# Performance work log

Hardware: AMD Instinct MI355X
Metric: run time of the kernel (lower is better)

## Reference

```python
import jax, jax.numpy as jnp
import numpy as np

D = 768; H = 6; HD = D // H; DFF = 2048
L = 512; S = 1024; B = 8
EPS = 1e-5
SCALE = 1.0 / float(np.sqrt(2 * D // H))  # fused q/k head_dim = 2*D/H (Conditional-DETR attention)


def _ln(x, g, b):
    m = x.mean(-1, keepdims=True)
    v = ((x - m) ** 2).mean(-1, keepdims=True)
    return (x - m) / jnp.sqrt(v + EPS) * g + b


def _lin(x, w, b):  # w: (out, in) torch convention
    return jnp.einsum('lbd,ed->lbe', x, w) + b


def _fuse(c, p):  # channel-concat per head: (L,B,D)x2 -> (L,B,H,2*HD)
    Lx, Bx, _ = c.shape
    c = c.reshape(Lx, Bx, H, HD)
    p = p.reshape(Lx, Bx, H, HD)
    return jnp.concatenate([c, p], axis=-1)


def _attn(q, k, v, ow, ob):
    # q:(L,B,H,2HD) k:(S,B,H,2HD) v:(S,B,D); out_proj maps vdim->vdim
    Lx, Bx = q.shape[0], q.shape[1]
    Sx = k.shape[0]
    vh = v.reshape(Sx, Bx, H, HD)
    scores = jnp.einsum('lbhd,sbhd->bhls', q * SCALE, k)
    w = jax.nn.softmax(scores, axis=-1)
    o = jnp.einsum('bhls,sbhe->lbhe', w, vh).reshape(Lx, Bx, D)
    return _lin(o, ow, ob), w.mean(axis=1)  # head-averaged attn weights (B,L,S)


def setup_inputs() -> dict:
    key = jax.random.key(0)
    ks = iter(jax.random.split(key, 64))
    d = {}
    d['tgt'] = jax.random.normal(next(ks), (L, B, D), jnp.float32)
    d['memory'] = jax.random.normal(next(ks), (S, B, D), jnp.float32)
    d['tgt_pos'] = jax.random.normal(next(ks), (L, B, D), jnp.float32)
    d['memory_pos'] = jax.random.normal(next(ks), (S, B, D), jnp.float32)
    d['tgt_pos2'] = jax.random.normal(next(ks), (L, B, D), jnp.float32)

    def W(shape):
        return jax.random.normal(next(ks), shape, jnp.float32) * 0.02

    for pre in ('sa', 'ca'):
        for nm in ('qc', 'qp', 'kc', 'kp', 'v', 'o'):
            d[f'{pre}_{nm}_w'] = W((D, D))
            d[f'{pre}_{nm}_b'] = jnp.zeros((D,), jnp.float32)
    d['ff1_w'] = W((DFF, D)); d['ff1_b'] = jnp.zeros((DFF,), jnp.float32)
    d['ff2_w'] = W((D, DFF)); d['ff2_b'] = jnp.zeros((D,), jnp.float32)
    for i in (1, 2, 3):
        d[f'ln{i}_g'] = jnp.ones((D,), jnp.float32)
        d[f'ln{i}_b'] = jnp.zeros((D,), jnp.float32)
    return d


def reference(tgt, memory, tgt_pos, memory_pos, tgt_pos2,
              sa_qc_w, sa_qc_b, sa_qp_w, sa_qp_b, sa_kc_w, sa_kc_b, sa_kp_w, sa_kp_b,
              sa_v_w, sa_v_b, sa_o_w, sa_o_b,
              ca_qc_w, ca_qc_b, ca_qp_w, ca_qp_b, ca_kc_w, ca_kc_b, ca_kp_w, ca_kp_b,
              ca_v_w, ca_v_b, ca_o_w, ca_o_b,
              ff1_w, ff1_b, ff2_w, ff2_b,
              ln1_g, ln1_b, ln2_g, ln2_b, ln3_g, ln3_b):
    # --- self attention (dropout = identity at inference) ---
    q = _fuse(_lin(tgt_pos, sa_qc_w, sa_qc_b), _lin(tgt, sa_qp_w, sa_qp_b))
    k = _fuse(_lin(tgt_pos, sa_kc_w, sa_kc_b), _lin(tgt, sa_kp_w, sa_kp_b))
    v = _lin(tgt, sa_v_w, sa_v_b)
    t2, self_att = _attn(q, k, v, sa_o_w, sa_o_b)
    t = _ln(tgt + t2, ln1_g, ln1_b)
    # --- cross attention ---
    q = _fuse(_lin(tgt_pos, ca_qc_w, ca_qc_b), _lin(t + tgt_pos2, ca_qp_w, ca_qp_b))
    k = _fuse(_lin(memory, ca_kc_w, ca_kc_b), _lin(memory_pos, ca_kp_w, ca_kp_b))
    v = _lin(memory_pos, ca_v_w, ca_v_b)
    t2, att = _attn(q, k, v, ca_o_w, ca_o_b)
    t = _ln(t + t2, ln2_g, ln2_b)
    # --- FFN + post-norm ---
    t2 = _lin(jax.nn.relu(_lin(t, ff1_w, ff1_b)), ff2_w, ff2_b)
    t = _ln(t + t2, ln3_g, ln3_b)
    return (t, att, self_att)
```

## Files before the change

### kernel.cpp

```cpp
#include <hip/hip_runtime.h>


typedef __bf16 bf16;
typedef __attribute__((ext_vector_type(8))) __bf16 bf16x8;
typedef __attribute__((ext_vector_type(4))) float f32x4;

#define D_MODEL 768
#define NH 6
#define HD 128
#define ROWSTRIDE (8 * D_MODEL)

__device__ inline void swz_xyz(int& x, int& y, int& z) {
    const int nx = gridDim.x, ny = gridDim.y;
    const int n = nx * ny * gridDim.z;
    const int flat = blockIdx.x + nx * (blockIdx.y + ny * blockIdx.z);
    const int t = (flat & 7) * (n >> 3) + (flat >> 3);
    x = t % nx;
    const int r = t / nx;
    y = r % ny;
    z = r / ny;
}

__device__ __forceinline__ void gld16(const bf16* g, bf16* l) {
    __builtin_amdgcn_global_load_lds(
        (const __attribute__((address_space(1))) unsigned int*)g,
        (__attribute__((address_space(3))) unsigned int*)l, 16, 0, 0);
}

__device__ inline bf16x8 ld8f(const float* p) {
    f32x4 a = *(const f32x4*)p, b = *(const f32x4*)(p + 4);
    bf16x8 r;
#pragma unroll
    for (int i = 0; i < 4; i++) { r[i] = (bf16)a[i]; r[i + 4] = (bf16)b[i]; }
    return r;
}
__device__ inline bf16x8 ld8bf(const bf16* p, const float* q) {
    bf16x8 x = *(const bf16x8*)p;
    f32x4 a = *(const f32x4*)q, b = *(const f32x4*)(q + 4);
    bf16x8 r;
#pragma unroll
    for (int i = 0; i < 4; i++) { r[i] = (bf16)((float)x[i] + a[i]); r[i + 4] = (bf16)((float)x[i + 4] + b[i]); }
    return r;
}
__device__ inline bf16x8 ld8ff(const float* p, const float* q) {
    f32x4 a = *(const f32x4*)p, b = *(const f32x4*)(p + 4);
    f32x4 c = *(const f32x4*)q, d = *(const f32x4*)(q + 4);
    bf16x8 r;
#pragma unroll
    for (int i = 0; i < 4; i++) { r[i] = (bf16)(a[i] + c[i]); r[i + 4] = (bf16)(b[i] + d[i]); }
    return r;
}

struct CvtJob { const float* src; const bf16* add; bf16* dst; int nvec; };
struct CvtJobs { CvtJob j[12]; };

__global__ __launch_bounds__(256) void cvt_multi(CvtJobs jobs)
{
    const CvtJob jb = jobs.j[blockIdx.y];
    const int stride = gridDim.x * 256;
    if (jb.add) {
        for (int i = blockIdx.x * 256 + threadIdx.x; i < jb.nvec; i += stride)
            *(bf16x8*)(jb.dst + (size_t)i * 8) = ld8bf(jb.add + (size_t)i * 8, jb.src + (size_t)i * 8);
    } else {
        for (int i = blockIdx.x * 256 + threadIdx.x; i < jb.nvec; i += stride)
            *(bf16x8*)(jb.dst + (size_t)i * 8) = ld8f(jb.src + (size_t)i * 8);
    }
}

struct JobB { const bf16* A; const bf16* W; const float* bias; bf16* C; int relu; };
struct JobsB { JobB j[5]; };

__global__ __launch_bounds__(256) void gemm_bb(
    JobsB jobs, int lda, int ldw, int ldc, int K)
{
    __shared__ __align__(16) bf16 As[128 * 32];
    __shared__ __align__(16) bf16 Bs[128 * 32];
    int bx, by, bz;
    swz_xyz(bx, by, bz);
    const JobB jb = jobs.j[bz];
    const int bm = by * 128, bn = bx * 128;
    const int tid = threadIdx.x;
    const int wave = tid >> 6, lane = tid & 63;
    const int wm = (wave >> 1) * 64, wn = (wave & 1) * 64;
    const int quad = lane >> 4, m16 = lane & 15;
    const int crow = lane >> 2, ccol = (lane & 3) * 8;
    const bf16* a0 = jb.A + (size_t)(bm + wave * 32 + crow) * lda + ccol;
    const bf16* a1 = a0 + (size_t)16 * lda;
    const bf16* w0 = jb.W + (size_t)(bn + wave * 32 + crow) * ldw + ccol;
    const bf16* w1 = w0 + (size_t)16 * ldw;
    bf16* lA = As + wave * 1024;
    bf16* lB = Bs + wave * 1024;
    f32x4 acc[4][4] = {};
    for (int k0 = 0; k0 < K; k0 += 32) {
        gld16(a0 + k0, lA);
        gld16(a1 + k0, lA + 512);
        gld16(w0 + k0, lB);
        gld16(w1 + k0, lB + 512);
        __syncthreads();
        bf16x8 af[4], bfr[4];
#pragma unroll
        for (int i = 0; i < 4; i++) {
            af[i]  = *(const bf16x8*)&As[(wm + i * 16 + m16) * 32 + quad * 8];
            bfr[i] = *(const bf16x8*)&Bs[(wn + i * 16 + m16) * 32 + quad * 8];
        }
#pragma unroll
        for (int i = 0; i < 4; i++)
#pragma unroll
            for (int j = 0; j < 4; j++)
                acc[i][j] = __builtin_amdgcn_mfma_f32_16x16x32_bf16(af[i], bfr[j], acc[i][j], 0, 0, 0);
        __syncthreads();
    }
#pragma unroll
    for (int j = 0; j < 4; j++) {
        const int col = bn + wn + j * 16 + m16;
        const float bv = jb.bias[col];
#pragma unroll
        for (int i = 0; i < 4; i++)
#pragma unroll
            for (int r = 0; r < 4; r++) {
                const int row = bm + wm + i * 16 + quad * 4 + r;
                float val = acc[i][j][r] + bv;
                if (jb.relu) val = fmaxf(val, 0.f);
                jb.C[(size_t)row * ldc + col] = (bf16)val;
            }
    }
}

__global__ __launch_bounds__(256) void gemm_sk_bb(
    const bf16* __restrict__ A, int lda, const bf16* __restrict__ W, int ldw,
    float* __restrict__ Cp, size_t cstride, int ldc, int Ks)
{
    __shared__ __align__(16) bf16 As[128 * 32];
    __shared__ __align__(16) bf16 Bs[128 * 32];
    int bx, by, bz;
    swz_xyz(bx, by, bz);
    const int bm = by * 128, bn = bx * 128;
    const int kbase = bz * Ks;
    const int tid = threadIdx.x;
    const int wave = tid >> 6, lane = tid & 63;
    const int wm = (wave >> 1) * 64, wn = (wave & 1) * 64;
    const int quad = lane >> 4, m16 = lane & 15;
    const int crow = lane >> 2, ccol = (lane & 3) * 8;
    const bf16* a0 = A + (size_t)(bm + wave * 32 + crow) * lda + kbase + ccol;
    const bf16* a1 = a0 + (size_t)16 * lda;
    const bf16* w0 = W + (size_t)(bn + wave * 32 + crow) * ldw + kbase + ccol;
    const bf16* w1 = w0 + (size_t)16 * ldw;
    bf16* lA = As + wave * 1024;
    bf16* lB = Bs + wave * 1024;
    f32x4 acc[4][4] = {};
    for (int k0 = 0; k0 < Ks; k0 += 32) {
        gld16(a0 + k0, lA);
        gld16(a1 + k0, lA + 512);
        gld16(w0 + k0, lB);
        gld16(w1 + k0, lB + 512);
        __syncthreads();
        bf16x8 af[4], bfr[4];
#pragma unroll
        for (int i = 0; i < 4; i++) {
            af[i]  = *(const bf16x8*)&As[(wm + i * 16 + m16) * 32 + quad * 8];
            bfr[i] = *(const bf16x8*)&Bs[(wn + i * 16 + m16) * 32 + quad * 8];
        }
#pragma unroll
        for (int i = 0; i < 4; i++)
#pragma unroll
            for (int j = 0; j < 4; j++)
                acc[i][j] = __builtin_amdgcn_mfma_f32_16x16x32_bf16(af[i], bfr[j], acc[i][j], 0, 0, 0);
        __syncthreads();
    }
    float* out = Cp + (size_t)bz * cstride;
#pragma unroll
    for (int j = 0; j < 4; j++) {
        const int col = bn + wn + j * 16 + m16;
#pragma unroll
        for (int i = 0; i < 4; i++)
#pragma unroll
            for (int r = 0; r < 4; r++) {
                const int row = bm + wm + i * 16 + quad * 4 + r;
                out[(size_t)row * ldc + col] = acc[i][j][r];
            }
    }
}

__global__ __launch_bounds__(256) void gemm_sk3(
    const float* __restrict__ A, const float* __restrict__ A2, int lda,
    const float* __restrict__ W, int ldw,
    float* __restrict__ Cp, size_t cstride, int ldc, int Ks)
{
    __shared__ __align__(16) bf16 As[128][40];
    __shared__ __align__(16) bf16 Bs[128][40];
    int bx, by, bz;
    swz_xyz(bx, by, bz);
    const int bm = by * 128, bn = bx * 128;
    const int kbase = bz * Ks;
    const int tid = threadIdx.x;
    const int wave = tid >> 6, lane = tid & 63;
    const int wm = (wave >> 1) * 64, wn = (wave & 1) * 64;
    const int quad = lane >> 4, m16 = lane & 15;
    const int srow = tid >> 2, scol = (tid & 3) * 8;
    f32x4 acc[4][4] = {};
    const size_t aoff0 = (size_t)(bm + srow) * lda + kbase + scol;
    const size_t aoff1 = aoff0 + (size_t)64 * lda;
    const size_t woff0 = (size_t)(bn + srow) * ldw + kbase + scol;
    const size_t woff1 = woff0 + (size_t)64 * ldw;
    bf16x8 a0, a1, b0, b1;
    a0 = ld8ff(A + aoff0, A2 + aoff0);
    a1 = ld8ff(A + aoff1, A2 + aoff1);
    b0 = ld8f(W + woff0);
    b1 = ld8f(W + woff1);
    for (int k0 = 0; k0 < Ks; k0 += 32) {
        *(bf16x8*)&As[srow][scol]      = a0;
        *(bf16x8*)&As[srow + 64][scol] = a1;
        *(bf16x8*)&Bs[srow][scol]      = b0;
        *(bf16x8*)&Bs[srow + 64][scol] = b1;
        __syncthreads();
        const int kn = k0 + 32;
        if (kn < Ks) {
            a0 = ld8ff(A + aoff0 + kn, A2 + aoff0 + kn);
            a1 = ld8ff(A + aoff1 + kn, A2 + aoff1 + kn);
            b0 = ld8f(W + woff0 + kn);
            b1 = ld8f(W + woff1 + kn);
        }
        bf16x8 af[4], bfr[4];
#pragma unroll
        for (int i = 0; i < 4; i++) {
            af[i]  = *(const bf16x8*)&As[wm + i * 16 + m16][quad * 8];
            bfr[i] = *(const bf16x8*)&Bs[wn + i * 16 + m16][quad * 8];
        }
#pragma unroll
        for (int i = 0; i < 4; i++)
#pragma unroll
            for (int j = 0; j < 4; j++)
                acc[i][j] = __builtin_amdgcn_mfma_f32_16x16x32_bf16(af[i], bfr[j], acc[i][j], 0, 0, 0);
        __syncthreads();
    }
    float* out = Cp + (size_t)bz * cstride;
#pragma unroll
    for (int j = 0; j < 4; j++) {
        const int col = bn + wn + j * 16 + m16;
#pragma unroll
        for (int i = 0; i < 4; i++)
#pragma unroll
            for (int r = 0; r < 4; r++) {
                const int row = bm + wm + i * 16 + quad * 4 + r;
                out[(size_t)row * ldc + col] = acc[i][j][r];
            }
    }
}

__global__ __launch_bounds__(256) void attn_scores(
    const bf16* __restrict__ qc, const bf16* __restrict__ qp,
    const bf16* __restrict__ kc, const bf16* __restrict__ kp,
    bf16* __restrict__ scores, int Lq, int S, float scale)
{
    __shared__ __align__(16) bf16 As[128 * 32];
    __shared__ __align__(16) bf16 Bs[128 * 32];
    int bx, by, bz;
    swz_xyz(bx, by, bz);
    const int bh = bz;
    const int b = bh / NH, h = bh % NH;
    const int bm = by * 128, bn = bx * 128;
    const int tid = threadIdx.x;
    const int wave = tid >> 6, lane = tid & 63;
    const int wm = (wave >> 1) * 64, wn = (wave & 1) * 64;
    const int quad = lane >> 4, m16 = lane & 15;
    const int crow = lane >> 2, ccol = (lane & 3) * 8;
    const size_t hb = (size_t)b * D_MODEL + h * HD;
    const size_t ar0 = (size_t)(bm + wave * 32 + crow) * ROWSTRIDE + hb + ccol;
    const size_t ar1 = ar0 + (size_t)16 * ROWSTRIDE;
    const size_t br0 = (size_t)(bn + wave * 32 + crow) * ROWSTRIDE + hb + ccol;
    const size_t br1 = br0 + (size_t)16 * ROWSTRIDE;
    bf16* lA = As + wave * 1024;
    bf16* lB = Bs + wave * 1024;
    f32x4 acc[4][4] = {};
    for (int k0 = 0; k0 < 256; k0 += 32) {
        const bf16* qsrc = (k0 < 128) ? qc : qp;
        const bf16* ksrc = (k0 < 128) ? kc : kp;
        const int kcol = k0 & 127;
        gld16(qsrc + ar0 + kcol, lA);
        gld16(qsrc + ar1 + kcol, lA + 512);
        gld16(ksrc + br0 + kcol, lB);
        gld16(ksrc + br1 + kcol, lB + 512);
        __syncthreads();
        bf16x8 af[4], bfr[4];
#pragma unroll
        for (int i = 0; i < 4; i++) {
            af[i]  = *(const bf16x8*)&As[(wm + i * 16 + m16) * 32 + quad * 8];
            bfr[i] = *(const bf16x8*)&Bs[(wn + i * 16 + m16) * 32 + quad * 8];
        }
#pragma unroll
        for (int i = 0; i < 4; i++)
#pragma unroll
            for (int j = 0; j < 4; j++)
                acc[i][j] = __builtin_amdgcn_mfma_f32_16x16x32_bf16(af[i], bfr[j], acc[i][j], 0, 0, 0);
        __syncthreads();
    }
    bf16* sb = scores + (size_t)bh * Lq * S;
#pragma unroll
    for (int i = 0; i < 4; i++)
#pragma unroll
        for (int j = 0; j < 4; j++)
#pragma unroll
            for (int r = 0; r < 4; r++)
                sb[(size_t)(bm + wm + i * 16 + quad * 4 + r) * S + bn + wn + j * 16 + m16]
                    = (bf16)(acc[i][j][r] * scale);
}

template <int N>
__global__ __launch_bounds__(256) void softmax_mean(
    bf16* __restrict__ scores, float* __restrict__ att, int Lq)
{
    const int S = N << 8;
    const int l = blockIdx.x, b = blockIdx.y;
    const int tid = threadIdx.x;
    __shared__ float red[4], red2[4];
    float macc[N];
#pragma unroll
    for (int i = 0; i < N; i++) macc[i] = 0.f;
    for (int h = 0; h < NH; h++) {
        bf16* p = scores + ((size_t)(b * NH + h) * Lq + l) * S;
        float vals[N];
        float mx = -1e30f;
#pragma unroll
        for (int i = 0; i < N; i++) { vals[i] = (float)p[tid + (i << 8)]; mx = fmaxf(mx, vals[i]); }
        for (int off = 32; off; off >>= 1) mx = fmaxf(mx, __shfl_xor(mx, off, 64));
        if ((tid & 63) == 0) red[tid >> 6] = mx;
        __syncthreads();
        mx = fmaxf(fmaxf(red[0], red[1]), fmaxf(red[2], red[3]));
        float sum = 0.f;
#pragma unroll
        for (int i = 0; i < N; i++) { vals[i] = __expf(vals[i] - mx); sum += vals[i]; }
        for (int off = 32; off; off >>= 1) sum += __shfl_xor(sum, off, 64);
        if ((tid & 63) == 0) red2[tid >> 6] = sum;
        __syncthreads();
        const float inv = 1.f / (red2[0] + red2[1] + red2[2] + red2[3]);
#pragma unroll
        for (int i = 0; i < N; i++) {
            const float w = vals[i] * inv;
            p[tid + (i << 8)] = (bf16)w;
            macc[i] += w;
        }
    }
    float* ao = att + ((size_t)b * Lq + l) * S;
#pragma unroll
    for (int i = 0; i < N; i++) ao[tid + (i << 8)] = macc[i] * (1.f / 6.f);
}

__global__ __launch_bounds__(256) void attn_pv_sk(
    const bf16* __restrict__ wsm, const bf16* __restrict__ v,
    float* __restrict__ Pv, size_t pstride, int Lq, int S)
{
    __shared__ __align__(16) bf16 As[128 * 32];
    __shared__ __align__(16) bf16 BsT[128][40];
    int bx, by, bz;
    swz_xyz(bx, by, bz);
    const int bh = bz;
    const int b = bh / NH, h = bh % NH;
    const int bm = bx * 128;
    const int kbase = by * (S >> 1);
    const int tid = threadIdx.x;
    const int wave = tid >> 6, lane = tid & 63;
    const int wm = (wave >> 1) * 64, wn = (wave & 1) * 64;
    const int quad = lane >> 4, m16 = lane & 15;
    const int crow = lane >> 2, ccol = (lane & 3) * 8;
    const int kk0 = tid >> 4, e0 = (tid & 15) * 8;
    f32x4 acc[4][4] = {};
    const bf16* wbase = wsm + (size_t)(bh * Lq + bm) * S + kbase;
    const size_t vb = (size_t)b * D_MODEL + h * HD;
    const bf16* a0 = wbase + (size_t)(wave * 32 + crow) * S + ccol;
    const bf16* a1 = a0 + (size_t)16 * S;
    bf16* lA = As + wave * 1024;
    bf16x8 v0, v1;
    v0 = *(const bf16x8*)(v + (size_t)(kbase + kk0) * ROWSTRIDE + vb + e0);
    v1 = *(const bf16x8*)(v + (size_t)(kbase + kk0 + 16) * ROWSTRIDE + vb + e0);
    for (int k0 = 0; k0 < (S >> 1); k0 += 32) {
        gld16(a0 + k0, lA);
        gld16(a1 + k0, lA + 512);
#pragma unroll
        for (int i = 0; i < 8; i++) { BsT[e0 + i][kk0] = v0[i]; BsT[e0 + i][kk0 + 16] = v1[i]; }
        __syncthreads();
        const int kn = k0 + 32;
        if (kn < (S >> 1)) {
            v0 = *(const bf16x8*)(v + (size_t)(kbase + kn + kk0) * ROWSTRIDE + vb + e0);
            v1 = *(const bf16x8*)(v + (size_t)(kbase + kn + kk0 + 16) * ROWSTRIDE + vb + e0);
        }
        bf16x8 af[4], bfr[4];
#pragma unroll
        for (int i = 0; i < 4; i++) {
            af[i]  = *(const bf16x8*)&As[(wm + i * 16 + m16) * 32 + quad * 8];
            bfr[i] = *(const bf16x8*)&BsT[wn + i * 16 + m16][quad * 8];
        }
#pragma unroll
        for (int i = 0; i < 4; i++)
#pragma unroll
            for (int j = 0; j < 4; j++)
                acc[i][j] = __builtin_amdgcn_mfma_f32_16x16x32_bf16(af[i], bfr[j], acc[i][j], 0, 0, 0);
        __syncthreads();
    }
    float* out = Pv + by * pstride;
#pragma unroll
    for (int i = 0; i < 4; i++)
#pragma unroll
        for (int j = 0; j < 4; j++)
#pragma unroll
            for (int r = 0; r < 4; r++)
                out[(size_t)(bm + wm + i * 16 + quad * 4 + r) * ROWSTRIDE + vb + wn + j * 16 + m16]
                    = acc[i][j][r];
}

template <int NP, typename TR, typename TO>
__global__ __launch_bounds__(256) void add_ln_p(
    const TR* __restrict__ resid, const float* __restrict__ P, size_t pstride,
    const float* __restrict__ xbias,
    const float* __restrict__ g, const float* __restrict__ be, TO* __restrict__ out)
{
    const size_t base = (size_t)blockIdx.x * D_MODEL;
    const int tid = threadIdx.x;
    float v[3];
#pragma unroll
    for (int i = 0; i < 3; i++) {
        const int c = tid + (i << 8);
        float x = xbias[c];
#pragma unroll
        for (int p = 0; p < NP; p++) x += P[p * pstride + base + c];
        v[i] = (float)resid[base + c] + x;
    }
    float s = v[0] + v[1] + v[2];
    float s2 = v[0] * v[0] + v[1] * v[1] + v[2] * v[2];
    for (int off = 32; off; off >>= 1) { s += __shfl_xor(s, off, 64); s2 += __shfl_xor(s2, off, 64); }
    __shared__ float rs[4], rs2[4];
    if ((tid & 63) == 0) { rs[tid >> 6] = s; rs2[tid >> 6] = s2; }
    __syncthreads();
    s = rs[0] + rs[1] + rs[2] + rs[3];
    s2 = rs2[0] + rs2[1] + rs2[2] + rs2[3];
    const float mean = s * (1.f / 768.f);
    const float var = s2 * (1.f / 768.f) - mean * mean;
    const float inv = rsqrtf(var + 1e-5f);
#pragma unroll
    for (int i = 0; i < 3; i++) {
        const int c = tid + (i << 8);
        out[base + c] = (TO)((v[i] - mean) * inv * g[c] + be[c]);
    }
}

extern "C" void kernel_launch(void* const* d_in, const int* in_sizes, int n_in,
                              void* d_out, int out_size, void* d_ws, size_t ws_size,
                              hipStream_t stream)
{
    const float* tgt        = (const float*)d_in[0];
    const float* memory     = (const float*)d_in[1];
    const float* tgt_pos    = (const float*)d_in[2];
    const float* memory_pos = (const float*)d_in[3];
    const float* tgt_pos2   = (const float*)d_in[4];
    const float *sa_w[6], *sa_b[6], *ca_w[6], *ca_b[6];
    for (int i = 0; i < 6; i++) {
        sa_w[i] = (const float*)d_in[5 + 2 * i];  sa_b[i] = (const float*)d_in[6 + 2 * i];
        ca_w[i] = (const float*)d_in[17 + 2 * i]; ca_b[i] = (const float*)d_in[18 + 2 * i];
    }
    const float* ff1_w = (const float*)d_in[29]; const float* ff1_b = (const float*)d_in[30];
    const float* ff2_w = (const float*)d_in[31]; const float* ff2_b = (const float*)d_in[32];
    const float* ln_g[3] = {(const float*)d_in[33], (const float*)d_in[35], (const float*)d_in[37]};
    const float* ln_b[3] = {(const float*)d_in[34], (const float*)d_in[36], (const float*)d_in[38]};

    char* ws = (char*)d_ws;
    bf16* qc  = (bf16*)(ws);
    bf16* qp  = (bf16*)(ws + 6291456);
    bf16* kc  = (bf16*)(ws + 12582912);
    bf16* kp  = (bf16*)(ws + 25165824);
    bf16* vv  = (bf16*)(ws + 37748736);
    bf16* t1  = (bf16*)(ws + 50331648);
    bf16* sc  = (bf16*)(ws + 56623104);
    const size_t PSTRIDE = 3145728;
    float* pv_sa = (float*)(ws + 81788928);
    float* pv_ca = (float*)(ws + 12582912);
    float* op    = (float*)(ws + 56623104);
    float* fp    = (float*)(ws + 56623104);
    bf16*  tca   = kc;
    bf16*  ffh   = kp;

    bf16* tgt_b    = sc;
    bf16* mem_b    = sc;
    bf16* mempos_b = sc + 6291456;
    bf16* wb       = (bf16*)d_out;
    const size_t WSTEP = 589824;
    bf16* tp_b   = (bf16*)((char*)d_out + 12582912);
    bf16* qpin_b = tp_b + 3145728;
    bf16* ff1b   = qc;
    bf16* ff2b   = qp;

    float* out_t    = (float*)d_out;
    float* out_att  = out_t + 3145728;
    float* out_satt = out_att + 4194304;

    const dim3 blk(256);
    const float SCALE = 0.0625f;

    {
        CvtJobs C = {};
        for (int i = 0; i < 5; i++) C.j[i] = {sa_w[i], nullptr, wb + i * WSTEP, 73728};
        for (int i = 0; i < 3; i++) C.j[5 + i] = {ca_w[2 + i], nullptr, wb + (5 + i) * WSTEP, 73728};
        C.j[8]  = {ca_w[0], nullptr, wb + 8 * WSTEP, 73728};
        C.j[9]  = {ca_w[1], nullptr, wb + 9 * WSTEP, 73728};
        C.j[10] = {tgt,     nullptr, tgt_b, 393216};
        C.j[11] = {tgt_pos, nullptr, tp_b,  393216};
        cvt_multi<<<dim3(288, 12), blk, 0, stream>>>(C);
    }

    {
        JobsB J = {};
        J.j[0] = {tp_b,  wb + 0 * WSTEP, sa_b[0], qc, 0};
        J.j[1] = {tgt_b, wb + 1 * WSTEP, sa_b[1], qp, 0};
        J.j[2] = {tp_b,  wb + 2 * WSTEP, sa_b[2], kc, 0};
        J.j[3] = {tgt_b, wb + 3 * WSTEP, sa_b[3], kp, 0};
        J.j[4] = {tgt_b, wb + 4 * WSTEP, sa_b[4], vv, 0};
        gemm_bb<<<dim3(6, 32, 5), blk, 0, stream>>>(J, 768, 768, 768, 768);
    }
    attn_scores<<<dim3(4, 4, 48), blk, 0, stream>>>(qc, qp, kc, kp, sc, 512, 512, SCALE);
    softmax_mean<2><<<dim3(512, 8), blk, 0, stream>>>(sc, out_satt, 512);
    attn_pv_sk<<<dim3(4, 2, 48), blk, 0, stream>>>(sc, vv, pv_sa, PSTRIDE, 512, 512);
    gemm_sk3<<<dim3(6, 32, 2), blk, 0, stream>>>(pv_sa, pv_sa + PSTRIDE, 768,
                                                 sa_w[5], 768, op, PSTRIDE, 768, 384);
    add_ln_p<2, float, bf16><<<dim3(4096), blk, 0, stream>>>(tgt, op, PSTRIDE, sa_b[5],
                                                             ln_g[0], ln_b[0], t1);

    {
        CvtJobs C = {};
        C.j[0] = {memory,     nullptr, mem_b,    786432};
        C.j[1] = {memory_pos, nullptr, mempos_b, 786432};
        C.j[2] = {tgt_pos2,   t1,      qpin_b,   393216};
        cvt_multi<<<dim3(288, 3), blk, 0, stream>>>(C);
    }

    {
        JobsB J = {};
        J.j[0] = {tp_b,   wb + 8 * WSTEP, ca_b[0], qc, 0};
        J.j[1] = {qpin_b, wb + 9 * WSTEP, ca_b[1], qp, 0};
        gemm_bb<<<dim3(6, 32, 2), blk, 0, stream>>>(J, 768, 768, 768, 768);
    }
    {
        JobsB J = {};
        J.j[0] = {mem_b,    wb + 5 * WSTEP, ca_b[2], kc, 0};
        J.j[1] = {mempos_b, wb + 6 * WSTEP, ca_b[3], kp, 0};
        J.j[2] = {mempos_b, wb + 7 * WSTEP, ca_b[4], vv, 0};
        gemm_bb<<<dim3(6, 64, 3), blk, 0, stream>>>(J, 768, 768, 768, 768);
    }
    attn_scores<<<dim3(8, 4, 48), blk, 0, stream>>>(qc, qp, kc, kp, sc, 512, 1024, SCALE);
    {
        CvtJobs C = {};
        C.j[0] = {ff1_w, nullptr, ff1b, 196608};
        C.j[1] = {ff2_w, nullptr, ff2b, 196608};
        cvt_multi<<<dim3(288, 2), blk, 0, stream>>>(C);
    }
    softmax_mean<4><<<dim3(512, 8), blk, 0, stream>>>(sc, out_att, 512);
    attn_pv_sk<<<dim3(4, 2, 48), blk, 0, stream>>>(sc, vv, pv_ca, PSTRIDE, 512, 1024);
    gemm_sk3<<<dim3(6, 32, 2), blk, 0, stream>>>(pv_ca, pv_ca + PSTRIDE, 768,
                                                 ca_w[5], 768, op, PSTRIDE, 768, 384);
    add_ln_p<2, bf16, bf16><<<dim3(4096), blk, 0, stream>>>(t1, op, PSTRIDE, ca_b[5],
                                                            ln_g[1], ln_b[1], tca);

    {
        JobsB J = {};
        J.j[0] = {tca, ff1b, ff1_b, ffh, 1};
        gemm_bb<<<dim3(16, 32, 1), blk, 0, stream>>>(J, 768, 768, 2048, 768);
    }
    gemm_sk_bb<<<dim3(6, 32, 4), blk, 0, stream>>>(ffh, 2048, ff2b, 2048,
                                                   fp, PSTRIDE, 768, 512);
    add_ln_p<4, bf16, float><<<dim3(4096), blk, 0, stream>>>(tca, fp, PSTRIDE, ff2_b,
                                                             ln_g[2], ln_b[2], out_t);
}
```

Before: 624.3 us.

## Double-buffer LDS in bf16 GEMMs and replace fp32 out-proj GEMM with cvt+bf16 GEMM

Adds two-stage LDS double buffering to gemm_bb, gemm_sk_bb and attn_scores, so the next K-tile's global-to-LDS load is issued before the current tile's MFMAs. This removes one barrier per iteration and aims to overlap load latency with compute. It also drops the fp32-input gemm_sk3 for the attention out-projections. Instead, a cvt_multi pass sums the split-K PV partials and converts them and the out-proj weight to bf16, then the async-load gemm_sk_bb runs. That costs an extra launch and an extra round trip through memory, and the doubled LDS may lower occupancy.

```diff
diff --git a/kernel.cpp b/kernel.cpp
--- a/kernel.cpp
+++ b/kernel.cpp
@@ -51,14 +51,17 @@
     return r;
 }
 
-struct CvtJob { const float* src; const bf16* add; bf16* dst; int nvec; };
+struct CvtJob { const float* src; const float* src2; const bf16* add; bf16* dst; int nvec; };
 struct CvtJobs { CvtJob j[12]; };
 
 __global__ __launch_bounds__(256) void cvt_multi(CvtJobs jobs)
 {
     const CvtJob jb = jobs.j[blockIdx.y];
     const int stride = gridDim.x * 256;
-    if (jb.add) {
+    if (jb.src2) {
+        for (int i = blockIdx.x * 256 + threadIdx.x; i < jb.nvec; i += stride)
+            *(bf16x8*)(jb.dst + (size_t)i * 8) = ld8ff(jb.src + (size_t)i * 8, jb.src2 + (size_t)i * 8);
+    } else if (jb.add) {
         for (int i = blockIdx.x * 256 + threadIdx.x; i < jb.nvec; i += stride)
             *(bf16x8*)(jb.dst + (size_t)i * 8) = ld8bf(jb.add + (size_t)i * 8, jb.src + (size_t)i * 8);
     } else {
@@ -73,8 +76,8 @@
 __global__ __launch_bounds__(256) void gemm_bb(
     JobsB jobs, int lda, int ldw, int ldc, int K)
 {
-    __shared__ __align__(16) bf16 As[128 * 32];
-    __shared__ __align__(16) bf16 Bs[128 * 32];
+    __shared__ __align__(16) bf16 As[2][128 * 32];
+    __shared__ __align__(16) bf16 Bs[2][128 * 32];
     int bx, by, bz;
     swz_xyz(bx, by, bz);
     const JobB jb = jobs.j[bz];
@@ -88,20 +91,31 @@
     const bf16* a1 = a0 + (size_t)16 * lda;
     const bf16* w0 = jb.W + (size_t)(bn + wave * 32 + crow) * ldw + ccol;
     const bf16* w1 = w0 + (size_t)16 * ldw;
-    bf16* lA = As + wave * 1024;
-    bf16* lB = Bs + wave * 1024;
+    const int wo = wave * 1024;
     f32x4 acc[4][4] = {};
+    gld16(a0, As[0] + wo);
+    gld16(a1, As[0] + wo + 512);
+    gld16(w0, Bs[0] + wo);
+    gld16(w1, Bs[0] + wo + 512);
+    __syncthreads();
+    int cur = 0;
     for (int k0 = 0; k0 < K; k0 += 32) {
-        gld16(a0 + k0, lA);
-        gld16(a1 + k0, lA + 512);
-        gld16(w0 + k0, lB);
-        gld16(w1 + k0, lB + 512);
-        __syncthreads();
+        const int kn = k0 + 32;
+        if (kn < K) {
+            bf16* dA = As[cur ^ 1] + wo;
+            bf16* dB = Bs[cur ^ 1] + wo;
+            gld16(a0 + kn, dA);
+            gld16(a1 + kn, dA + 512);
+            gld16(w0 + kn, dB);
+            gld16(w1 + kn, dB + 512);
+        }
+        const bf16* rA = As[cur];
+        const bf16* rB = Bs[cur];
         bf16x8 af[4], bfr[4];
 #pragma unroll
         for (int i = 0; i < 4; i++) {
-            af[i]  = *(const bf16x8*)&As[(wm + i * 16 + m16) * 32 + quad * 8];
-            bfr[i] = *(const bf16x8*)&Bs[(wn + i * 16 + m16) * 32 + quad * 8];
+            af[i]  = *(const bf16x8*)&rA[(wm + i * 16 + m16) * 32 + quad * 8];
+            bfr[i] = *(const bf16x8*)&rB[(wn + i * 16 + m16) * 32 + quad * 8];
         }
 #pragma unroll
         for (int i = 0; i < 4; i++)
@@ -109,6 +123,7 @@
             for (int j = 0; j < 4; j++)
                 acc[i][j] = __builtin_amdgcn_mfma_f32_16x16x32_bf16(af[i], bfr[j], acc[i][j], 0, 0, 0);
         __syncthreads();
+        cur ^= 1;
     }
 #pragma unroll
     for (int j = 0; j < 4; j++) {
@@ -130,8 +145,8 @@
     const bf16* __restrict__ A, int lda, const bf16* __restrict__ W, int ldw,
     float* __restrict__ Cp, size_t cstride, int ldc, int Ks)
 {
-    __shared__ __align__(16) bf16 As[128 * 32];
-    __shared__ __align__(16) bf16 Bs[128 * 32];
+    __shared__ __align__(16) bf16 As[2][128 * 32];
+    __shared__ __align__(16) bf16 Bs[2][128 * 32];
     int bx, by, bz;
     swz_xyz(bx, by, bz);
     const int bm = by * 128, bn = bx * 128;
@@ -145,20 +160,31 @@
     const bf16* a1 = a0 + (size_t)16 * lda;
     const bf16* w0 = W + (size_t)(bn + wave * 32 + crow) * ldw + kbase + ccol;
     const bf16* w1 = w0 + (size_t)16 * ldw;
-    bf16* lA = As + wave * 1024;
-    bf16* lB = Bs + wave * 1024;
+    const int wo = wave * 1024;
     f32x4 acc[4][4] = {};
+    gld16(a0, As[0] + wo);
+    gld16(a1, As[0] + wo + 512);
+    gld16(w0, Bs[0] + wo);
+    gld16(w1, Bs[0] + wo + 512);
+    __syncthreads();
+    int cur = 0;
     for (int k0 = 0; k0 < Ks; k0 += 32) {
-        gld16(a0 + k0, lA);
-        gld16(a1 + k0, lA + 512);
-        gld16(w0 + k0, lB);
-        gld16(w1 + k0, lB + 512);
-        __syncthreads();
+        const int kn = k0 + 32;
+        if (kn < Ks) {
+            bf16* dA = As[cur ^ 1] + wo;
+            bf16* dB = Bs[cur ^ 1] + wo;
+            gld16(a0 + kn, dA);
+            gld16(a1 + kn, dA + 512);
+            gld16(w0 + kn, dB);
+            gld16(w1 + kn, dB + 512);
+        }
+        const bf16* rA = As[cur];
+        const bf16* rB = Bs[cur];
         bf16x8 af[4], bfr[4];
 #pragma unroll
         for (int i = 0; i < 4; i++) {
-            af[i]  = *(const bf16x8*)&As[(wm + i * 16 + m16) * 32 + quad * 8];
-            bfr[i] = *(const bf16x8*)&Bs[(wn + i * 16 + m16) * 32 + quad * 8];
+            af[i]  = *(const bf16x8*)&rA[(wm + i * 16 + m16) * 32 + quad * 8];
+            bfr[i] = *(const bf16x8*)&rB[(wn + i * 16 + m16) * 32 + quad * 8];
         }
 #pragma unroll
         for (int i = 0; i < 4; i++)
@@ -166,6 +192,7 @@
             for (int j = 0; j < 4; j++)
                 acc[i][j] = __builtin_amdgcn_mfma_f32_16x16x32_bf16(af[i], bfr[j], acc[i][j], 0, 0, 0);
         __syncthreads();
+        cur ^= 1;
     }
     float* out = Cp + (size_t)bz * cstride;
 #pragma unroll
@@ -181,79 +208,13 @@
     }
 }
 
-__global__ __launch_bounds__(256) void gemm_sk3(
-    const float* __restrict__ A, const float* __restrict__ A2, int lda,
-    const float* __restrict__ W, int ldw,
-    float* __restrict__ Cp, size_t cstride, int ldc, int Ks)
-{
-    __shared__ __align__(16) bf16 As[128][40];
-    __shared__ __align__(16) bf16 Bs[128][40];
-    int bx, by, bz;
-    swz_xyz(bx, by, bz);
-    const int bm = by * 128, bn = bx * 128;
-    const int kbase = bz * Ks;
-    const int tid = threadIdx.x;
-    const int wave = tid >> 6, lane = tid & 63;
-    const int wm = (wave >> 1) * 64, wn = (wave & 1) * 64;
-    const int quad = lane >> 4, m16 = lane & 15;
-    const int srow = tid >> 2, scol = (tid & 3) * 8;
-    f32x4 acc[4][4] = {};
-    const size_t aoff0 = (size_t)(bm + srow) * lda + kbase + scol;
-    const size_t aoff1 = aoff0 + (size_t)64 * lda;
-    const size_t woff0 = (size_t)(bn + srow) * ldw + kbase + scol;
-    const size_t woff1 = woff0 + (size_t)64 * ldw;
-    bf16x8 a0, a1, b0, b1;
-    a0 = ld8ff(A + aoff0, A2 + aoff0);
-    a1 = ld8ff(A + aoff1, A2 + aoff1);
-    b0 = ld8f(W + woff0);
-    b1 = ld8f(W + woff1);
-    for (int k0 = 0; k0 < Ks; k0 += 32) {
-        *(bf16x8*)&As[srow][scol]      = a0;
-        *(bf16x8*)&As[srow + 64][scol] = a1;
-        *(bf16x8*)&Bs[srow][scol]      = b0;
-        *(bf16x8*)&Bs[srow + 64][scol] = b1;
-        __syncthreads();
-        const int kn = k0 + 32;
-        if (kn < Ks) {
-            a0 = ld8ff(A + aoff0 + kn, A2 + aoff0 + kn);
-            a1 = ld8ff(A + aoff1 + kn, A2 + aoff1 + kn);
-            b0 = ld8f(W + woff0 + kn);
-            b1 = ld8f(W + woff1 + kn);
-        }
-        bf16x8 af[4], bfr[4];
-#pragma unroll
-        for (int i = 0; i < 4; i++) {
-            af[i]  = *(const bf16x8*)&As[wm + i * 16 + m16][quad * 8];
-            bfr[i] = *(const bf16x8*)&Bs[wn + i * 16 + m16][quad * 8];
-        }
-#pragma unroll
-        for (int i = 0; i < 4; i++)
-#pragma unroll
-            for (int j = 0; j < 4; j++)
-                acc[i][j] = __builtin_amdgcn_mfma_f32_16x16x32_bf16(af[i], bfr[j], acc[i][j], 0, 0, 0);
-        __syncthreads();
-    }
-    float* out = Cp + (size_t)bz * cstride;
-#pragma unroll
-    for (int j = 0; j < 4; j++) {
-        const int col = bn + wn + j * 16 + m16;
-#pragma unroll
-        for (int i = 0; i < 4; i++)
-#pragma unroll
-            for (int r = 0; r < 4; r++) {
-                const int row = bm + wm + i * 16 + quad * 4 + r;
-                out[(size_t)row * ldc + col] = acc[i][j][r];
-            }
-    }
-}
-
 __global__ __launch_bounds__(256) void attn_scores(
     const bf16* __restrict__ qc, const bf16* __restrict__ qp,
     const bf16* __restrict__ kc, const bf16* __restrict__ kp,
     bf16* __restrict__ scores, int Lq, int S, float scale)
 {
-    __shared__ __align__(16) bf16 As[128 * 32];
-    __shared__ __align__(16) bf16 Bs[128 * 32];
+    __shared__ __align__(16) bf16 As[2][128 * 32];
+    __shared__ __align__(16) bf16 Bs[2][128 * 32];
     int bx, by, bz;
     swz_xyz(bx, by, bz);
     const int bh = bz;
@@ -269,23 +230,34 @@
     const size_t ar1 = ar0 + (size_t)16 * ROWSTRIDE;
     const size_t br0 = (size_t)(bn + wave * 32 + crow) * ROWSTRIDE + hb + ccol;
     const size_t br1 = br0 + (size_t)16 * ROWSTRIDE;
-    bf16* lA = As + wave * 1024;
-    bf16* lB = Bs + wave * 1024;
+    const int wo = wave * 1024;
     f32x4 acc[4][4] = {};
+    gld16(qc + ar0, As[0] + wo);
+    gld16(qc + ar1, As[0] + wo + 512);
+    gld16(kc + br0, Bs[0] + wo);
+    gld16(kc + br1, Bs[0] + wo + 512);
+    __syncthreads();
+    int cur = 0;
     for (int k0 = 0; k0 < 256; k0 += 32) {
-        const bf16* qsrc = (k0 < 128) ? qc : qp;
-        const bf16* ksrc = (k0 < 128) ? kc : kp;
-        const int kcol = k0 & 127;
-        gld16(qsrc + ar0 + kcol, lA);
-        gld16(qsrc + ar1 + kcol, lA + 512);
-        gld16(ksrc + br0 + kcol, lB);
-        gld16(ksrc + br1 + kcol, lB + 512);
-        __syncthreads();
+        const int kn = k0 + 32;
+        if (kn < 256) {
+            const bf16* qsrc = (kn < 128) ? qc : qp;
+            const bf16* ksrc = (kn < 128) ? kc : kp;
+            const int kcol = kn & 127;
+            bf16* dA = As[cur ^ 1] + wo;
+            bf16* dB = Bs[cur ^ 1] + wo;
+            gld16(qsrc + ar0 + kcol, dA);
+            gld16(qsrc + ar1 + kcol, dA + 512);
+            gld16(ksrc + br0 + kcol, dB);
+            gld16(ksrc + br1 + kcol, dB + 512);
+        }
+        const bf16* rA = As[cur];
+        const bf16* rB = Bs[cur];
         bf16x8 af[4], bfr[4];
 #pragma unroll
         for (int i = 0; i < 4; i++) {
-            af[i]  = *(const bf16x8*)&As[(wm + i * 16 + m16) * 32 + quad * 8];
-            bfr[i] = *(const bf16x8*)&Bs[(wn + i * 16 + m16) * 32 + quad * 8];
+            af[i]  = *(const bf16x8*)&rA[(wm + i * 16 + m16) * 32 + quad * 8];
+            bfr[i] = *(const bf16x8*)&rB[(wn + i * 16 + m16) * 32 + quad * 8];
         }
 #pragma unroll
         for (int i = 0; i < 4; i++)
@@ -293,6 +265,7 @@
             for (int j = 0; j < 4; j++)
                 acc[i][j] = __builtin_amdgcn_mfma_f32_16x16x32_bf16(af[i], bfr[j], acc[i][j], 0, 0, 0);
         __syncthreads();
+        cur ^= 1;
     }
     bf16* sb = scores + (size_t)bh * Lq * S;
 #pragma unroll
@@ -486,6 +459,10 @@
     bf16* qpin_b = tp_b + 3145728;
     bf16* ff1b   = qc;
     bf16* ff2b   = qp;
+    bf16* savA   = kc;
+    bf16* saw5b  = kc + 3145728;
+    bf16* cavA   = vv;
+    bf16* caw5b  = vv + 3145728;
 
     float* out_t    = (float*)d_out;
     float* out_att  = out_t + 3145728;
@@ -496,12 +473,12 @@
 
     {
         CvtJobs C = {};
-        for (int i = 0; i < 5; i++) C.j[i] = {sa_w[i], nullptr, wb + i * WSTEP, 73728};
-        for (int i = 0; i < 3; i++) C.j[5 + i] = {ca_w[2 + i], nullptr, wb + (5 + i) * WSTEP, 73728};
-        C.j[8]  = {ca_w[0], nullptr, wb + 8 * WSTEP, 73728};
-        C.j[9]  = {ca_w[1], nullptr, wb + 9 * WSTEP, 73728};
-        C.j[10] = {tgt,     nullptr, tgt_b, 393216};
-        C.j[11] = {tgt_pos, nullptr, tp_b,  393216};
+        for (int i = 0; i < 5; i++) C.j[i] = {sa_w[i], nullptr, nullptr, wb + i * WSTEP, 73728};
+        for (int i = 0; i < 3; i++) C.j[5 + i] = {ca_w[2 + i], nullptr, nullptr, wb + (5 + i) * WSTEP, 73728};
+        C.j[8]  = {ca_w[0], nullptr, nullptr, wb + 8 * WSTEP, 73728};
+        C.j[9]  = {ca_w[1], nullptr, nullptr, wb + 9 * WSTEP, 73728};
+        C.j[10] = {tgt,     nullptr, nullptr, tgt_b, 393216};
+        C.j[11] = {tgt_pos, nullptr, nullptr, tp_b,  393216};
         cvt_multi<<<dim3(288, 12), blk, 0, stream>>>(C);
     }
 
@@ -517,16 +494,22 @@
     attn_scores<<<dim3(4, 4, 48), blk, 0, stream>>>(qc, qp, kc, kp, sc, 512, 512, SCALE);
     softmax_mean<2><<<dim3(512, 8), blk, 0, stream>>>(sc, out_satt, 512);
     attn_pv_sk<<<dim3(4, 2, 48), blk, 0, stream>>>(sc, vv, pv_sa, PSTRIDE, 512, 512);
-    gemm_sk3<<<dim3(6, 32, 2), blk, 0, stream>>>(pv_sa, pv_sa + PSTRIDE, 768,
-                                                 sa_w[5], 768, op, PSTRIDE, 768, 384);
+    {
+        CvtJobs C = {};
+        C.j[0] = {pv_sa, pv_sa + PSTRIDE, nullptr, savA,  393216};
+        C.j[1] = {sa_w[5], nullptr,       nullptr, saw5b, 73728};
+        cvt_multi<<<dim3(288, 2), blk, 0, stream>>>(C);
+    }
+    gemm_sk_bb<<<dim3(6, 32, 2), blk, 0, stream>>>(savA, 768, saw5b, 768,
+                                                   op, PSTRIDE, 768, 384);
     add_ln_p<2, float, bf16><<<dim3(4096), blk, 0, stream>>>(tgt, op, PSTRIDE, sa_b[5],
                                                              ln_g[0], ln_b[0], t1);
 
     {
         CvtJobs C = {};
-        C.j[0] = {memory,     nullptr, mem_b,    786432};
-        C.j[1] = {memory_pos, nullptr, mempos_b, 786432};
-        C.j[2] = {tgt_pos2,   t1,      qpin_b,   393216};
+        C.j[0] = {memory,     nullptr, nullptr, mem_b,    786432};
+        C.j[1] = {memory_pos, nullptr, nullptr, mempos_b, 786432};
+        C.j[2] = {tgt_pos2,   nullptr, t1,      qpin_b,   393216};
         cvt_multi<<<dim3(288, 3), blk, 0, stream>>>(C);
     }
 
@@ -546,14 +529,20 @@
     attn_scores<<<dim3(8, 4, 48), blk, 0, stream>>>(qc, qp, kc, kp, sc, 512, 1024, SCALE);
     {
         CvtJobs C = {};
-        C.j[0] = {ff1_w, nullptr, ff1b, 196608};
-        C.j[1] = {ff2_w, nullptr, ff2b, 196608};
+        C.j[0] = {ff1_w, nullptr, nullptr, ff1b, 196608};
+        C.j[1] = {ff2_w, nullptr, nullptr, ff2b, 196608};
         cvt_multi<<<dim3(288, 2), blk, 0, stream>>>(C);
     }
     softmax_mean<4><<<dim3(512, 8), blk, 0, stream>>>(sc, out_att, 512);
     attn_pv_sk<<<dim3(4, 2, 48), blk, 0, stream>>>(sc, vv, pv_ca, PSTRIDE, 512, 1024);
-    gemm_sk3<<<dim3(6, 32, 2), blk, 0, stream>>>(pv_ca, pv_ca + PSTRIDE, 768,
-                                                 ca_w[5], 768, op, PSTRIDE, 768, 384);
+    {
+        CvtJobs C = {};
+        C.j[0] = {pv_ca, pv_ca + PSTRIDE, nullptr, cavA,  393216};
+        C.j[1] = {ca_w[5], nullptr,       nullptr, caw5b, 73728};
+        cvt_multi<<<dim3(288, 2), blk, 0, stream>>>(C);
+    }
+    gemm_sk_bb<<<dim3(6, 32, 2), blk, 0, stream>>>(cavA, 768, caw5b, 768,
+                                                   op, PSTRIDE, 768, 384);
     add_ln_p<2, bf16, bf16><<<dim3(4096), blk, 0, stream>>>(t1, op, PSTRIDE, ca_b[5],
                                                             ln_g[1], ln_b[1], tca);
 
```

Measured after the change: 613.3 us. No clear change (-1.8%).
